# Kernel tuning notes

Measured on AMD Instinct MI355X. Metric: run time of the kernel, lower is better.

## Reference

```python
import jax, jax.numpy as jnp
import numpy as np

T, B, I, H, O = 64, 1024, 64, 256, 1


def setup_inputs() -> dict:
    key = jax.random.key(0)
    ks = jax.random.split(key, 8)
    k = 1.0 / np.sqrt(H)  # torch RNN/Linear default init bound
    u = lambda kk, sh: jax.random.uniform(kk, sh, jnp.float32, -k, k)
    return {
        'data': jax.random.normal(ks[0], (T, B, I), jnp.float32),
        'nine_target_index': jax.random.randint(ks[1], (B, 9), 0, B + 1),  # B == outside-target pad row
        'haven_flag': 0,
        'h0': jnp.zeros((B, H), jnp.float32),  # init_hidden (layer dim squeezed)
        'W_ih': u(ks[2], (H, I)),
        'W_hh': u(ks[3], (H, H)),
        'b_ih': u(ks[4], (H,)),
        'b_hh': u(ks[5], (H,)),
        'W_lin': u(ks[6], (O, 2 * H)),
        'b_lin': u(ks[7], (O,)),
    }


def _forward(data, nine_target_index, haven_flag, h0, W_ih, W_hh, b_ih, b_hh, W_lin, b_lin):
    # --- vanilla relu RNN over time (seq-first layout, 1 layer) ---
    def step(h, x):
        h = jax.nn.relu(x @ W_ih.T + b_ih + h @ W_hh.T + b_hh)
        return h, h
    _, hs = jax.lax.scan(step, h0, data)          # (T, B, H) == hidden_output

    # Original code detaches hidden states before the numpy attention round-trip:
    hd = jax.lax.stop_gradient(hs)
    # pad batch dim with one zero 'outside target' row, then gather 3x3 neighborhoods
    h_pad = jnp.concatenate([hd, jnp.zeros((hd.shape[0], 1, H), hd.dtype)], axis=1)  # (T, B+1, H)
    gathered = h_pad[:, nine_target_index]        # (T, B, 9, H)  past_ht per timestep
    if haven_flag == 1:
        gathered = jnp.concatenate(
            [gathered, jnp.zeros(gathered.shape[:2] + (1, H), gathered.dtype)], axis=2)

    # scores[i, j, b, n] = <past_ht[j, b, n, :], ht[i, b, :]>  (query also detached in original)
    scores = jnp.einsum('jbnh,ibh->ijbn', gathered, hd)
    attn = jax.nn.softmax(scores, axis=-1)        # softmax over the 9 neighbors (dim=2 in torch)
    Tn = hs.shape[0]
    # c[i] = sum over strictly-past timesteps j < i of the attention-weighted neighbor states
    mask = jnp.tril(jnp.ones((Tn, Tn), attn.dtype), -1)       # mask[i, j] = 1 iff j < i
    attn_m = attn * mask[:, :, None, None]
    c_rest = jnp.einsum('ijbn,jbnh->ibh', attn_m, gathered)   # (T, B, H)
    # i == 0 with LAG=='ALL': c[0] = hidden_output[0] (NOT detached in original)
    c = jnp.concatenate([hs[:1], c_rest[1:]], axis=0)

    concat = jnp.concatenate([c, hs], axis=-1)    # (T, B, 2H)
    pred = jax.nn.relu(concat @ W_lin.T + b_lin)  # (T, B, O)
    return pred, attn


def reference(data, nine_target_index, haven_flag, h0, W_ih, W_hh, b_ih, b_hh, W_lin, b_lin):
    return _forward(data, nine_target_index, haven_flag, h0, W_ih, W_hh, b_ih, b_hh, W_lin, b_lin)
```

## Files before the change

### kernel.cpp

```cpp
#include <hip/hip_runtime.h>

#define T_ 64
#define B_ 1024
#define I_ 64
#define H_ 256

typedef short bf16x8 __attribute__((ext_vector_type(8)));
typedef float f32x4 __attribute__((ext_vector_type(4)));

#define MFMA16(a, b, c) __builtin_amdgcn_mfma_f32_16x16x32_bf16((a), (b), (c), 0, 0, 0)

__device__ __forceinline__ float bf2f(unsigned short u) {
    union { unsigned int i; float f; } x;
    x.i = ((unsigned int)u) << 16;
    return x.f;
}
__device__ __forceinline__ unsigned short f2bf(float f) {
    union { float f; unsigned int i; } x;
    x.f = f;
    unsigned int u = x.i;
    unsigned int r = u + 0x7FFFu + ((u >> 16) & 1u);
    return (unsigned short)(r >> 16);
}
__device__ __forceinline__ void split8(const float* p, bf16x8& hi, bf16x8& lo) {
    for (int q = 0; q < 8; ++q) {
        float f = p[q];
        unsigned short h1 = f2bf(f);
        hi[q] = (short)h1;
        lo[q] = (short)f2bf(f - bf2f(h1));
    }
}

__global__ __launch_bounds__(512, 2) void rnn_kernel(
    const float* __restrict__ data,
    const float* __restrict__ h0,
    const float* __restrict__ Wih, const float* __restrict__ Whh,
    const float* __restrict__ bih, const float* __restrict__ bhh,
    unsigned short* __restrict__ hsHi, unsigned short* __restrict__ hsLo)
{
    __shared__ unsigned short hbuf[2][2][16 * 264];
    __shared__ float bsum[H_];

    const int tid  = threadIdx.x;
    const int lane = tid & 63;
    const int w    = tid >> 6;
    const int quad = lane >> 4;
    const int l15  = lane & 15;
    const int b0   = blockIdx.x * 16;

    bf16x8 whhH[2][8], whhL[2][8], wihH[2][2], wihL[2][2];
    for (int it = 0; it < 2; ++it) {
        int n = (w * 2 + it) * 16 + l15;
        for (int kc = 0; kc < 8; ++kc)
            split8(Whh + (size_t)n * H_ + kc * 32 + quad * 8, whhH[it][kc], whhL[it][kc]);
        for (int kx = 0; kx < 2; ++kx)
            split8(Wih + (size_t)n * I_ + kx * 32 + quad * 8, wihH[it][kx], wihL[it][kx]);
    }

    if (tid < H_) bsum[tid] = bih[tid] + bhh[tid];
    {
        int r  = tid >> 5;
        int hh = (tid & 31) * 8;
        const float* src = h0 + (size_t)(b0 + r) * H_ + hh;
        for (int q = 0; q < 8; ++q) {
            float f = src[q];
            unsigned short hi = f2bf(f);
            hbuf[0][0][r * 264 + hh + q] = hi;
            hbuf[0][1][r * 264 + hh + q] = f2bf(f - bf2f(hi));
        }
    }
    __syncthreads();

    int cur = 0;
    for (int t = 0; t < T_; ++t) {
        f32x4 acc[2];
        acc[0] = (f32x4){0.f, 0.f, 0.f, 0.f};
        acc[1] = (f32x4){0.f, 0.f, 0.f, 0.f};

        for (int kx = 0; kx < 2; ++kx) {
            bf16x8 xhi, xlo;
            split8(data + ((size_t)t * B_ + b0 + l15) * I_ + kx * 32 + quad * 8, xhi, xlo);
            for (int it = 0; it < 2; ++it) {
                acc[it] = MFMA16(xhi, wihH[it][kx], acc[it]);
                acc[it] = MFMA16(xhi, wihL[it][kx], acc[it]);
                acc[it] = MFMA16(xlo, wihH[it][kx], acc[it]);
            }
        }
        for (int kc = 0; kc < 8; ++kc) {
            bf16x8 ahi = *(const bf16x8*)&hbuf[cur][0][l15 * 264 + kc * 32 + quad * 8];
            bf16x8 alo = *(const bf16x8*)&hbuf[cur][1][l15 * 264 + kc * 32 + quad * 8];
            for (int it = 0; it < 2; ++it) {
                acc[it] = MFMA16(ahi, whhH[it][kc], acc[it]);
                acc[it] = MFMA16(ahi, whhL[it][kc], acc[it]);
                acc[it] = MFMA16(alo, whhH[it][kc], acc[it]);
            }
        }

        int nxt = cur ^ 1;
        for (int it = 0; it < 2; ++it) {
            int h = (w * 2 + it) * 16 + l15;
            float bs = bsum[h];
            for (int reg = 0; reg < 4; ++reg) {
                int r = quad * 4 + reg;
                float v = acc[it][reg] + bs;
                v = fmaxf(v, 0.f);
                unsigned short hi = f2bf(v);
                unsigned short lo = f2bf(v - bf2f(hi));
                hbuf[nxt][0][r * 264 + h] = hi;
                hbuf[nxt][1][r * 264 + h] = lo;
            }
        }
        __syncthreads();
        {
            int r  = tid >> 5;
            int hc = (tid & 31) * 8;
            size_t g = ((size_t)t * B_ + b0 + r) * H_ + hc;
            *(bf16x8*)(hsHi + g) = *(const bf16x8*)&hbuf[nxt][0][r * 264 + hc];
            *(bf16x8*)(hsLo + g) = *(const bf16x8*)&hbuf[nxt][1][r * 264 + hc];
        }
        cur = nxt;
    }
}

__global__ __launch_bounds__(256) void attn_kernel(
    const unsigned short* __restrict__ hsHi,
    const unsigned short* __restrict__ hsLo,
    const int* __restrict__ nti,
    const float* __restrict__ Wlin,
    const float* __restrict__ blin,
    float* __restrict__ outPred,
    float* __restrict__ outAttn)
{
    __shared__ unsigned short GpH[32 * 264];
    __shared__ unsigned short GpL[32 * 264];
    __shared__ unsigned short GpT[256 * 40];
    __shared__ unsigned short Pb[64 * 40];
    __shared__ float wl[2 * H_];
    __shared__ float predc[64];
    __shared__ int   sidx[9];
    __shared__ float blin_s;

    const int tid  = threadIdx.x;
    const int lane = tid & 63;
    const int w    = tid >> 6;
    const int quad = lane >> 4;
    const int l15  = lane & 15;
    const int b    = blockIdx.x;

    for (int e = tid; e < 2 * H_; e += 256) wl[e] = Wlin[e];
    if (tid == 0) blin_s = blin[0];
    if (tid < 9) sidx[tid] = nti[b * 9 + tid];
    for (int e = tid; e < 14 * 264; e += 256) {
        int rr = e / 264, c = e % 264;
        int row = (rr < 7) ? (9 + rr) : (18 + rr);
        GpH[row * 264 + c] = 0;
        GpL[row * 264 + c] = 0;
    }
    for (int e = tid; e < 256 * 14; e += 256) {
        int h = e / 14, c = 18 + e % 14;
        GpT[h * 40 + c] = 0;
    }
    for (int e = tid; e < 64 * 14; e += 256) {
        int i = e / 14, c = 18 + e % 14;
        Pb[i * 40 + c] = 0;
    }

    bf16x8 af[8], afl[8];
    {
        size_t base = ((size_t)(w * 16 + l15) * B_ + b) * H_;
        for (int kc = 0; kc < 8; ++kc) {
            af[kc]  = *(const bf16x8*)(hsHi + base + kc * 32 + quad * 8);
            afl[kc] = *(const bf16x8*)(hsLo + base + kc * 32 + quad * 8);
        }
    }
    f32x4 acc[16];
    for (int nt = 0; nt < 16; ++nt) acc[nt] = (f32x4){0.f, 0.f, 0.f, 0.f};
    __syncthreads();

    for (int p = 0; p < 32; ++p) {
        int j0 = 2 * p;
        for (int n = w; n < 9; n += 4) {
            int bi = sidx[n];
            ushort4 vh0, vl0, vh1, vl1;
            if (bi < B_) {
                size_t base0 = ((size_t)j0 * B_ + bi) * H_;
                size_t base1 = base0 + (size_t)B_ * H_;
                vh0 = ((const ushort4*)(hsHi + base0))[lane];
                vl0 = ((const ushort4*)(hsLo + base0))[lane];
                vh1 = ((const ushort4*)(hsHi + base1))[lane];
                vl1 = ((const ushort4*)(hsLo + base1))[lane];
            } else {
                vh0.x=vh0.y=vh0.z=vh0.w=0; vl0.x=vl0.y=vl0.z=vl0.w=0;
                vh1.x=vh1.y=vh1.z=vh1.w=0; vl1.x=vl1.y=vl1.z=vl1.w=0;
            }
            *(ushort4*)&GpH[n * 264 + lane * 4]        = vh0;
            *(ushort4*)&GpL[n * 264 + lane * 4]        = vl0;
            *(ushort4*)&GpH[(16 + n) * 264 + lane * 4] = vh1;
            *(ushort4*)&GpL[(16 + n) * 264 + lane * 4] = vl1;
            unsigned short h0v[4] = {vh0.x, vh0.y, vh0.z, vh0.w};
            unsigned short h1v[4] = {vh1.x, vh1.y, vh1.z, vh1.w};
            for (int q = 0; q < 4; ++q) {
                ushort2 pr2; pr2.x = h0v[q]; pr2.y = h1v[q];
                *(ushort2*)&GpT[(lane * 4 + q) * 40 + 2 * n] = pr2;
            }
        }
        __syncthreads();

        for (int jslot = 0; jslot < 2; ++jslot) {
            int j = j0 + jslot;
            f32x4 s = (f32x4){0.f, 0.f, 0.f, 0.f};
            for (int kc = 0; kc < 8; ++kc) {
                bf16x8 aH = *(const bf16x8*)&GpH[(jslot * 16 + l15) * 264 + kc * 32 + quad * 8];
                bf16x8 aL = *(const bf16x8*)&GpL[(jslot * 16 + l15) * 264 + kc * 32 + quad * 8];
                s = MFMA16(aH, af[kc],  s);
                s = MFMA16(aH, afl[kc], s);
                s = MFMA16(aL, af[kc],  s);
            }
            int i = w * 16 + l15;
            int nvalid = (quad < 2) ? 4 : ((quad == 2) ? 1 : 0);
            float mp = -1e30f;
            for (int r = 0; r < 4; ++r) if (r < nvalid) mp = fmaxf(mp, s[r]);
            mp = fmaxf(mp, __shfl_xor(mp, 16, 64));
            mp = fmaxf(mp, __shfl_xor(mp, 32, 64));
            float e[4], sp = 0.f;
            for (int r = 0; r < 4; ++r) {
                e[r] = (r < nvalid) ? __expf(s[r] - mp) : 0.f;
                sp += e[r];
            }
            sp += __shfl_xor(sp, 16, 64);
            sp += __shfl_xor(sp, 32, 64);
            float inv = 1.f / sp;
            for (int r = 0; r < 4; ++r) {
                if (r < nvalid) {
                    int n = quad * 4 + r;
                    float pr = e[r] * inv;
                    outAttn[(((size_t)i * T_ + j) * B_ + b) * 9 + n] = pr;
                    unsigned short pm = (j < i) ? f2bf(pr) : (unsigned short)0;
                    Pb[i * 40 + 2 * n + jslot] = pm;
                }
            }
        }

        {
            bf16x8 afp = *(const bf16x8*)&Pb[(w * 16 + l15) * 40 + quad * 8];
            for (int nt = 0; nt < 16; ++nt) {
                bf16x8 bfg = *(const bf16x8*)&GpT[(nt * 16 + l15) * 40 + quad * 8];
                acc[nt] = MFMA16(afp, bfg, acc[nt]);
            }
        }
        __syncthreads();
    }

    float hw1 = 0.f, hw2 = 0.f;
    for (int kc = 0; kc < 8; ++kc) {
        for (int jj = 0; jj < 8; ++jj) {
            float hv = bf2f((unsigned short)af[kc][jj]) + bf2f((unsigned short)afl[kc][jj]);
            int h = kc * 32 + quad * 8 + jj;
            hw1 += hv * wl[h];
            hw2 += hv * wl[H_ + h];
        }
    }
    hw1 += __shfl_xor(hw1, 16, 64); hw1 += __shfl_xor(hw1, 32, 64);
    hw2 += __shfl_xor(hw2, 16, 64); hw2 += __shfl_xor(hw2, 32, 64);

    for (int reg = 0; reg < 4; ++reg) {
        float cp = 0.f;
        for (int nt = 0; nt < 16; ++nt)
            cp += acc[nt][reg] * wl[nt * 16 + l15];
        for (int m = 8; m >= 1; m >>= 1) cp += __shfl_xor(cp, m, 16);
        if (l15 == 0) predc[w * 16 + quad * 4 + reg] = cp;
    }
    __syncthreads();
    if (lane < 16) {
        int i = w * 16 + lane;
        float v = predc[i] + hw2 + ((i == 0) ? hw1 : 0.f) + blin_s;
        v = fmaxf(v, 0.f);
        outPred[(size_t)i * B_ + b] = v;
    }
}

extern "C" void kernel_launch(void* const* d_in, const int* in_sizes, int n_in,
                              void* d_out, int out_size, void* d_ws, size_t ws_size,
                              hipStream_t stream) {
    (void)in_sizes; (void)n_in; (void)out_size; (void)ws_size;
    const float* data = (const float*)d_in[0];
    const int*   nti  = (const int*)d_in[1];
    const float* h0   = (const float*)d_in[3];
    const float* Wih  = (const float*)d_in[4];
    const float* Whh  = (const float*)d_in[5];
    const float* bih  = (const float*)d_in[6];
    const float* bhh  = (const float*)d_in[7];
    const float* Wlin = (const float*)d_in[8];
    const float* blin = (const float*)d_in[9];

    unsigned short* ws = (unsigned short*)d_ws;
    unsigned short* hsHi = ws;
    unsigned short* hsLo = ws + (size_t)T_ * B_ * H_;

    float* outPred = (float*)d_out;
    float* outAttn = (float*)d_out + (size_t)T_ * B_;

    rnn_kernel<<<dim3(64), dim3(512), 0, stream>>>(data, h0, Wih, Whh, bih, bhh, hsHi, hsLo);
    attn_kernel<<<dim3(1024), dim3(256), 0, stream>>>(hsHi, hsLo, nti, Wlin, blin,
                                                      outPred, outAttn);
}
```

Before: 620.9 us.

## Restructure RNN to 4 waves with x prefetch; software-pipeline attention gathers

The RNN kernel drops from 8 to 4 waves per block, so each wave now computes four 16-column tiles. It also prefetches the next timestep's input into registers and interleaves independent MFMAs for more instruction-level parallelism. The attention kernel issues the next pair's neighbour gathers into registers before computing the current pair, packs the gather rows more tightly in LDS, and reads Wlin from global instead of LDS, all to cut LDS footprint and allow more blocks per CU. The catch is higher register pressure, since all of Whh is now held in fewer waves, plus fewer waves available to hide latency in the serial RNN loop.

```diff
diff --git a/kernel.cpp b/kernel.cpp
--- a/kernel.cpp
+++ b/kernel.cpp
@@ -23,6 +23,7 @@
     return (unsigned short)(r >> 16);
 }
 __device__ __forceinline__ void split8(const float* p, bf16x8& hi, bf16x8& lo) {
+#pragma unroll
     for (int q = 0; q < 8; ++q) {
         float f = p[q];
         unsigned short h1 = f2bf(f);
@@ -31,7 +32,7 @@
     }
 }
 
-__global__ __launch_bounds__(512, 2) void rnn_kernel(
+__global__ __launch_bounds__(256, 1) void rnn_kernel(
     const float* __restrict__ data,
     const float* __restrict__ h0,
     const float* __restrict__ Wih, const float* __restrict__ Whh,
@@ -48,21 +49,25 @@
     const int l15  = lane & 15;
     const int b0   = blockIdx.x * 16;
 
-    bf16x8 whhH[2][8], whhL[2][8], wihH[2][2], wihL[2][2];
-    for (int it = 0; it < 2; ++it) {
-        int n = (w * 2 + it) * 16 + l15;
+    bf16x8 whhH[4][8], whhL[4][8], wihH[4][2], wihL[4][2];
+#pragma unroll
+    for (int it = 0; it < 4; ++it) {
+        int n = (w * 4 + it) * 16 + l15;
+#pragma unroll
         for (int kc = 0; kc < 8; ++kc)
             split8(Whh + (size_t)n * H_ + kc * 32 + quad * 8, whhH[it][kc], whhL[it][kc]);
+#pragma unroll
         for (int kx = 0; kx < 2; ++kx)
             split8(Wih + (size_t)n * I_ + kx * 32 + quad * 8, wihH[it][kx], wihL[it][kx]);
     }
 
-    if (tid < H_) bsum[tid] = bih[tid] + bhh[tid];
+    bsum[tid] = bih[tid] + bhh[tid];
     {
-        int r  = tid >> 5;
-        int hh = (tid & 31) * 8;
+        int r  = tid >> 4;
+        int hh = (tid & 15) * 16;
         const float* src = h0 + (size_t)(b0 + r) * H_ + hh;
-        for (int q = 0; q < 8; ++q) {
+#pragma unroll
+        for (int q = 0; q < 16; ++q) {
             float f = src[q];
             unsigned short hi = f2bf(f);
             hbuf[0][0][r * 264 + hh + q] = hi;
@@ -71,35 +76,62 @@
     }
     __syncthreads();
 
+    float xf[16];
+    {
+        const float* dp = data + ((size_t)(b0 + l15)) * I_ + quad * 8;
+#pragma unroll
+        for (int q = 0; q < 8; ++q) { xf[q] = dp[q]; xf[8 + q] = dp[32 + q]; }
+    }
+
     int cur = 0;
     for (int t = 0; t < T_; ++t) {
-        f32x4 acc[2];
-        acc[0] = (f32x4){0.f, 0.f, 0.f, 0.f};
-        acc[1] = (f32x4){0.f, 0.f, 0.f, 0.f};
-
+        bf16x8 xhi[2], xlo[2];
+#pragma unroll
+        for (int kx = 0; kx < 2; ++kx)
+#pragma unroll
+            for (int q = 0; q < 8; ++q) {
+                float f = xf[kx * 8 + q];
+                unsigned short h1 = f2bf(f);
+                xhi[kx][q] = (short)h1;
+                xlo[kx][q] = (short)f2bf(f - bf2f(h1));
+            }
+        if (t + 1 < T_) {
+            const float* dp = data + ((size_t)(t + 1) * B_ + b0 + l15) * I_ + quad * 8;
+#pragma unroll
+            for (int q = 0; q < 8; ++q) { xf[q] = dp[q]; xf[8 + q] = dp[32 + q]; }
+        }
+
+        f32x4 acc[4];
+#pragma unroll
+        for (int it = 0; it < 4; ++it) acc[it] = (f32x4){0.f, 0.f, 0.f, 0.f};
+
+#pragma unroll
         for (int kx = 0; kx < 2; ++kx) {
-            bf16x8 xhi, xlo;
-            split8(data + ((size_t)t * B_ + b0 + l15) * I_ + kx * 32 + quad * 8, xhi, xlo);
-            for (int it = 0; it < 2; ++it) {
-                acc[it] = MFMA16(xhi, wihH[it][kx], acc[it]);
-                acc[it] = MFMA16(xhi, wihL[it][kx], acc[it]);
-                acc[it] = MFMA16(xlo, wihH[it][kx], acc[it]);
-            }
-        }
+#pragma unroll
+            for (int it = 0; it < 4; ++it) acc[it] = MFMA16(xhi[kx], wihH[it][kx], acc[it]);
+#pragma unroll
+            for (int it = 0; it < 4; ++it) acc[it] = MFMA16(xhi[kx], wihL[it][kx], acc[it]);
+#pragma unroll
+            for (int it = 0; it < 4; ++it) acc[it] = MFMA16(xlo[kx], wihH[it][kx], acc[it]);
+        }
+#pragma unroll
         for (int kc = 0; kc < 8; ++kc) {
             bf16x8 ahi = *(const bf16x8*)&hbuf[cur][0][l15 * 264 + kc * 32 + quad * 8];
             bf16x8 alo = *(const bf16x8*)&hbuf[cur][1][l15 * 264 + kc * 32 + quad * 8];
-            for (int it = 0; it < 2; ++it) {
-                acc[it] = MFMA16(ahi, whhH[it][kc], acc[it]);
-                acc[it] = MFMA16(ahi, whhL[it][kc], acc[it]);
-                acc[it] = MFMA16(alo, whhH[it][kc], acc[it]);
-            }
+#pragma unroll
+            for (int it = 0; it < 4; ++it) acc[it] = MFMA16(ahi, whhH[it][kc], acc[it]);
+#pragma unroll
+            for (int it = 0; it < 4; ++it) acc[it] = MFMA16(ahi, whhL[it][kc], acc[it]);
+#pragma unroll
+            for (int it = 0; it < 4; ++it) acc[it] = MFMA16(alo, whhH[it][kc], acc[it]);
         }
 
         int nxt = cur ^ 1;
-        for (int it = 0; it < 2; ++it) {
-            int h = (w * 2 + it) * 16 + l15;
+#pragma unroll
+        for (int it = 0; it < 4; ++it) {
+            int h = (w * 4 + it) * 16 + l15;
             float bs = bsum[h];
+#pragma unroll
             for (int reg = 0; reg < 4; ++reg) {
                 int r = quad * 4 + reg;
                 float v = acc[it][reg] + bs;
@@ -112,17 +144,19 @@
         }
         __syncthreads();
         {
-            int r  = tid >> 5;
-            int hc = (tid & 31) * 8;
+            int r  = tid >> 4;
+            int hc = (tid & 15) * 16;
             size_t g = ((size_t)t * B_ + b0 + r) * H_ + hc;
-            *(bf16x8*)(hsHi + g) = *(const bf16x8*)&hbuf[nxt][0][r * 264 + hc];
-            *(bf16x8*)(hsLo + g) = *(const bf16x8*)&hbuf[nxt][1][r * 264 + hc];
+            *(bf16x8*)(hsHi + g)     = *(const bf16x8*)&hbuf[nxt][0][r * 264 + hc];
+            *(bf16x8*)(hsHi + g + 8) = *(const bf16x8*)&hbuf[nxt][0][r * 264 + hc + 8];
+            *(bf16x8*)(hsLo + g)     = *(const bf16x8*)&hbuf[nxt][1][r * 264 + hc];
+            *(bf16x8*)(hsLo + g + 8) = *(const bf16x8*)&hbuf[nxt][1][r * 264 + hc + 8];
         }
         cur = nxt;
     }
 }
 
-__global__ __launch_bounds__(256) void attn_kernel(
+__global__ __launch_bounds__(256, 3) void attn_kernel(
     const unsigned short* __restrict__ hsHi,
     const unsigned short* __restrict__ hsLo,
     const int* __restrict__ nti,
@@ -131,11 +165,10 @@
     float* __restrict__ outPred,
     float* __restrict__ outAttn)
 {
-    __shared__ unsigned short GpH[32 * 264];
-    __shared__ unsigned short GpL[32 * 264];
+    __shared__ unsigned short GpH[25 * 264];
+    __shared__ unsigned short GpL[25 * 264];
     __shared__ unsigned short GpT[256 * 40];
     __shared__ unsigned short Pb[64 * 40];
-    __shared__ float wl[2 * H_];
     __shared__ float predc[64];
     __shared__ int   sidx[9];
     __shared__ float blin_s;
@@ -147,15 +180,8 @@
     const int l15  = lane & 15;
     const int b    = blockIdx.x;
 
-    for (int e = tid; e < 2 * H_; e += 256) wl[e] = Wlin[e];
     if (tid == 0) blin_s = blin[0];
     if (tid < 9) sidx[tid] = nti[b * 9 + tid];
-    for (int e = tid; e < 14 * 264; e += 256) {
-        int rr = e / 264, c = e % 264;
-        int row = (rr < 7) ? (9 + rr) : (18 + rr);
-        GpH[row * 264 + c] = 0;
-        GpL[row * 264 + c] = 0;
-    }
     for (int e = tid; e < 256 * 14; e += 256) {
         int h = e / 14, c = 18 + e % 14;
         GpT[h * 40 + c] = 0;
@@ -168,50 +194,77 @@
     bf16x8 af[8], afl[8];
     {
         size_t base = ((size_t)(w * 16 + l15) * B_ + b) * H_;
+#pragma unroll
         for (int kc = 0; kc < 8; ++kc) {
             af[kc]  = *(const bf16x8*)(hsHi + base + kc * 32 + quad * 8);
             afl[kc] = *(const bf16x8*)(hsLo + base + kc * 32 + quad * 8);
         }
     }
     f32x4 acc[16];
+#pragma unroll
     for (int nt = 0; nt < 16; ++nt) acc[nt] = (f32x4){0.f, 0.f, 0.f, 0.f};
     __syncthreads();
 
+    ushort4 gh0[3], gl0[3], gh1[3], gl1[3];
+
+#define ISSUE_GATHER(P)                                                        \
+    {                                                                          \
+        int j0g = 2 * (P);                                                     \
+        _Pragma("unroll")                                                      \
+        for (int c = 0; c < 3; ++c) {                                          \
+            int n = w + 4 * c;                                                 \
+            if (n < 9) {                                                       \
+                int bi = sidx[n];                                              \
+                if (bi < B_) {                                                 \
+                    size_t base0 = ((size_t)j0g * B_ + bi) * H_;               \
+                    size_t base1 = base0 + (size_t)B_ * H_;                    \
+                    gh0[c] = ((const ushort4*)(hsHi + base0))[lane];           \
+                    gl0[c] = ((const ushort4*)(hsLo + base0))[lane];           \
+                    gh1[c] = ((const ushort4*)(hsHi + base1))[lane];           \
+                    gl1[c] = ((const ushort4*)(hsLo + base1))[lane];           \
+                } else {                                                       \
+                    gh0[c].x=gh0[c].y=gh0[c].z=gh0[c].w=0;                     \
+                    gl0[c].x=gl0[c].y=gl0[c].z=gl0[c].w=0;                     \
+                    gh1[c].x=gh1[c].y=gh1[c].z=gh1[c].w=0;                     \
+                    gl1[c].x=gl1[c].y=gl1[c].z=gl1[c].w=0;                     \
+                }                                                              \
+            }                                                                  \
+        }                                                                      \
+    }
+
+    ISSUE_GATHER(0);
+
     for (int p = 0; p < 32; ++p) {
         int j0 = 2 * p;
-        for (int n = w; n < 9; n += 4) {
-            int bi = sidx[n];
-            ushort4 vh0, vl0, vh1, vl1;
-            if (bi < B_) {
-                size_t base0 = ((size_t)j0 * B_ + bi) * H_;
-                size_t base1 = base0 + (size_t)B_ * H_;
-                vh0 = ((const ushort4*)(hsHi + base0))[lane];
-                vl0 = ((const ushort4*)(hsLo + base0))[lane];
-                vh1 = ((const ushort4*)(hsHi + base1))[lane];
-                vl1 = ((const ushort4*)(hsLo + base1))[lane];
-            } else {
-                vh0.x=vh0.y=vh0.z=vh0.w=0; vl0.x=vl0.y=vl0.z=vl0.w=0;
-                vh1.x=vh1.y=vh1.z=vh1.w=0; vl1.x=vl1.y=vl1.z=vl1.w=0;
-            }
-            *(ushort4*)&GpH[n * 264 + lane * 4]        = vh0;
-            *(ushort4*)&GpL[n * 264 + lane * 4]        = vl0;
-            *(ushort4*)&GpH[(16 + n) * 264 + lane * 4] = vh1;
-            *(ushort4*)&GpL[(16 + n) * 264 + lane * 4] = vl1;
-            unsigned short h0v[4] = {vh0.x, vh0.y, vh0.z, vh0.w};
-            unsigned short h1v[4] = {vh1.x, vh1.y, vh1.z, vh1.w};
-            for (int q = 0; q < 4; ++q) {
-                ushort2 pr2; pr2.x = h0v[q]; pr2.y = h1v[q];
-                *(ushort2*)&GpT[(lane * 4 + q) * 40 + 2 * n] = pr2;
-            }
-        }
+        if (p) __syncthreads();
+#pragma unroll
+        for (int c = 0; c < 3; ++c) {
+            int n = w + 4 * c;
+            if (n < 9) {
+                *(ushort4*)&GpH[n * 264 + lane * 4]       = gh0[c];
+                *(ushort4*)&GpL[n * 264 + lane * 4]       = gl0[c];
+                *(ushort4*)&GpH[(9 + n) * 264 + lane * 4] = gh1[c];
+                *(ushort4*)&GpL[(9 + n) * 264 + lane * 4] = gl1[c];
+                unsigned short h0v[4] = {gh0[c].x, gh0[c].y, gh0[c].z, gh0[c].w};
+                unsigned short h1v[4] = {gh1[c].x, gh1[c].y, gh1[c].z, gh1[c].w};
+#pragma unroll
+                for (int q = 0; q < 4; ++q) {
+                    ushort2 pr2; pr2.x = h0v[q]; pr2.y = h1v[q];
+                    *(ushort2*)&GpT[(lane * 4 + q) * 40 + 2 * n] = pr2;
+                }
+            }
+        }
+        if (p < 31) ISSUE_GATHER(p + 1);
         __syncthreads();
 
+#pragma unroll
         for (int jslot = 0; jslot < 2; ++jslot) {
             int j = j0 + jslot;
             f32x4 s = (f32x4){0.f, 0.f, 0.f, 0.f};
+#pragma unroll
             for (int kc = 0; kc < 8; ++kc) {
-                bf16x8 aH = *(const bf16x8*)&GpH[(jslot * 16 + l15) * 264 + kc * 32 + quad * 8];
-                bf16x8 aL = *(const bf16x8*)&GpL[(jslot * 16 + l15) * 264 + kc * 32 + quad * 8];
+                bf16x8 aH = *(const bf16x8*)&GpH[(jslot * 9 + l15) * 264 + kc * 32 + quad * 8];
+                bf16x8 aL = *(const bf16x8*)&GpL[(jslot * 9 + l15) * 264 + kc * 32 + quad * 8];
                 s = MFMA16(aH, af[kc],  s);
                 s = MFMA16(aH, afl[kc], s);
                 s = MFMA16(aL, af[kc],  s);
@@ -219,10 +272,12 @@
             int i = w * 16 + l15;
             int nvalid = (quad < 2) ? 4 : ((quad == 2) ? 1 : 0);
             float mp = -1e30f;
+#pragma unroll
             for (int r = 0; r < 4; ++r) if (r < nvalid) mp = fmaxf(mp, s[r]);
             mp = fmaxf(mp, __shfl_xor(mp, 16, 64));
             mp = fmaxf(mp, __shfl_xor(mp, 32, 64));
             float e[4], sp = 0.f;
+#pragma unroll
             for (int r = 0; r < 4; ++r) {
                 e[r] = (r < nvalid) ? __expf(s[r] - mp) : 0.f;
                 sp += e[r];
@@ -230,6 +285,7 @@
             sp += __shfl_xor(sp, 16, 64);
             sp += __shfl_xor(sp, 32, 64);
             float inv = 1.f / sp;
+#pragma unroll
             for (int r = 0; r < 4; ++r) {
                 if (r < nvalid) {
                     int n = quad * 4 + r;
@@ -243,30 +299,34 @@
 
         {
             bf16x8 afp = *(const bf16x8*)&Pb[(w * 16 + l15) * 40 + quad * 8];
+#pragma unroll
             for (int nt = 0; nt < 16; ++nt) {
                 bf16x8 bfg = *(const bf16x8*)&GpT[(nt * 16 + l15) * 40 + quad * 8];
                 acc[nt] = MFMA16(afp, bfg, acc[nt]);
             }
         }
-        __syncthreads();
     }
 
     float hw1 = 0.f, hw2 = 0.f;
+#pragma unroll
     for (int kc = 0; kc < 8; ++kc) {
+#pragma unroll
         for (int jj = 0; jj < 8; ++jj) {
             float hv = bf2f((unsigned short)af[kc][jj]) + bf2f((unsigned short)afl[kc][jj]);
             int h = kc * 32 + quad * 8 + jj;
-            hw1 += hv * wl[h];
-            hw2 += hv * wl[H_ + h];
+            hw1 += hv * Wlin[h];
+            hw2 += hv * Wlin[H_ + h];
         }
     }
     hw1 += __shfl_xor(hw1, 16, 64); hw1 += __shfl_xor(hw1, 32, 64);
     hw2 += __shfl_xor(hw2, 16, 64); hw2 += __shfl_xor(hw2, 32, 64);
 
+#pragma unroll
     for (int reg = 0; reg < 4; ++reg) {
         float cp = 0.f;
+#pragma unroll
         for (int nt = 0; nt < 16; ++nt)
-            cp += acc[nt][reg] * wl[nt * 16 + l15];
+            cp += acc[nt][reg] * Wlin[nt * 16 + l15];
         for (int m = 8; m >= 1; m >>= 1) cp += __shfl_xor(cp, m, 16);
         if (l15 == 0) predc[w * 16 + quad * 4 + reg] = cp;
     }
@@ -300,7 +360,7 @@
     float* outPred = (float*)d_out;
     float* outAttn = (float*)d_out + (size_t)T_ * B_;
 
-    rnn_kernel<<<dim3(64), dim3(512), 0, stream>>>(data, h0, Wih, Whh, bih, bhh, hsHi, hsLo);
+    rnn_kernel<<<dim3(64), dim3(256), 0, stream>>>(data, h0, Wih, Whh, bih, bhh, hsHi, hsLo);
     attn_kernel<<<dim3(1024), dim3(256), 0, stream>>>(hsHi, hsLo, nti, Wlin, blin,
                                                       outPred, outAttn);
 }
```

Measured after the change: 1.041 ms. 67.7% more time.
